# Performance work log

Hardware: AMD Instinct MI355X
Metric: run time of the kernel (lower is better)

Reference implementation:

```python
import jax, jax.numpy as jnp
import numpy as np

D_MODEL = 2048
NUM_HEADS = 16
HEAD_DIM = D_MODEL // NUM_HEADS  # 128
ROPE_BASE = 10000.0
B, L = 2, 2048


def _rope_tables(seq_len, head_dim, base):
    # inv_freq over even dims; cos/sin tables of shape (seq_len, head_dim)
    inv_freq = 1.0 / (base ** (jnp.arange(0, head_dim, 2, dtype=jnp.float32) / head_dim))
    t = jnp.arange(seq_len, dtype=jnp.float32)
    freqs = jnp.einsum('l,d->ld', t, inv_freq)          # (L, head_dim/2)
    emb = jnp.concatenate([freqs, freqs], axis=-1)       # (L, head_dim)
    return jnp.cos(emb), jnp.sin(emb)


def _apply_rope(x, cos, sin):
    # x: (B, H, L, d); rotate-half convention
    d = x.shape[-1]
    x1, x2 = x[..., : d // 2], x[..., d // 2:]
    rotated = jnp.concatenate([-x2, x1], axis=-1)
    return x * cos + rotated * sin


def setup_inputs() -> dict:
    key = jax.random.key(0)
    k0, k1, k2 = jax.random.split(key, 3)
    query = jax.random.normal(k0, (B, L, D_MODEL), dtype=jnp.float32)
    W_qkv = jax.random.normal(k1, (3 * D_MODEL, D_MODEL), dtype=jnp.float32) * 0.02
    b_qkv = jnp.zeros((3 * D_MODEL,), dtype=jnp.float32)
    W_out = jax.random.normal(k2, (D_MODEL, D_MODEL), dtype=jnp.float32) * 0.02
    b_out = jnp.zeros((D_MODEL,), dtype=jnp.float32)
    return {"query": query, "W_qkv": W_qkv, "b_qkv": b_qkv, "W_out": W_out, "b_out": b_out}


def reference(query, W_qkv, b_qkv, W_out, b_out):
    Bq, Lq, _ = query.shape
    # fused QKV projection (single matmul)
    qkv = jnp.einsum('bld,ed->ble', query, W_qkv) + b_qkv  # (B, L, 3D)
    q, k, v = jnp.split(qkv, 3, axis=-1)

    def shape_heads(x):
        return x.reshape(Bq, Lq, NUM_HEADS, HEAD_DIM).transpose(0, 2, 1, 3)  # (B,H,L,d)

    q, k, v = shape_heads(q), shape_heads(k), shape_heads(v)

    cos, sin = _rope_tables(Lq, HEAD_DIM, ROPE_BASE)
    q = _apply_rope(q, cos, sin)
    k = _apply_rope(k, cos, sin)

    scale = 1.0 / jnp.sqrt(jnp.asarray(HEAD_DIM, dtype=q.dtype))
    scores = jnp.einsum('bhqd,bhkd->bhqk', q, k) * scale  # (B,H,L,L)
    causal = jnp.tril(jnp.ones((Lq, Lq), dtype=bool))
    scores = jnp.where(causal, scores, jnp.finfo(scores.dtype).min)
    probs = jax.nn.softmax(scores, axis=-1)
    attn = jnp.einsum('bhqk,bhkd->bhqd', probs, v)        # (B,H,L,d)

    out = attn.transpose(0, 2, 1, 3).reshape(Bq, Lq, D_MODEL)
    return jnp.einsum('bld,ed->ble', out, W_out) + b_out
```

## Files before the change

### kernel.cpp

```cpp
#include <hip/hip_runtime.h>

typedef unsigned short u16;
typedef unsigned int u32;
typedef __bf16 bf16x8 __attribute__((ext_vector_type(8)));
typedef float f32x4 __attribute__((ext_vector_type(4)));

__device__ __forceinline__ u16 f2b(float f) {
  u32 u = __float_as_uint(f);
  u32 r = (u + 0x7fffu + ((u >> 16) & 1u)) >> 16;
  return (u16)r;
}
__device__ __forceinline__ float b2f(u16 v) {
  return __uint_as_float(((u32)v) << 16);
}

__global__ __launch_bounds__(256) void convert_f32_bf16(
    const float4* __restrict__ in, ushort4* __restrict__ out, int n4) {
  int i = blockIdx.x * 256 + threadIdx.x;
  if (i >= n4) return;
  float4 f = in[i];
  ushort4 o;
  o.x = f2b(f.x); o.y = f2b(f.y); o.z = f2b(f.z); o.w = f2b(f.w);
  out[i] = o;
}

template <int OUT_BF16>
__global__ __launch_bounds__(256) void gemm_bt(
    const u16* __restrict__ A, const u16* __restrict__ B,
    const float* __restrict__ bias, void* __restrict__ Cv,
    int M, int N, int K) {
  __shared__ __align__(16) u16 As[128 * 32];
  __shared__ __align__(16) u16 Bs[128 * 32];
  const int tid = threadIdx.x;
  const int lane = tid & 63;
  const int wave = tid >> 6;
  const int m0 = blockIdx.y * 128;
  const int n0 = blockIdx.x * 128;
  const int wm = (wave & 1) * 64;
  const int wn = (wave >> 1) * 64;
  f32x4 acc[4][4] = {};

  const int sr = lane >> 2, sc = lane & 3;
  const int cs = ((sc - (sr >> 1)) & 3) * 16;
  const int srow0 = wave * 32 + sr;
  const int fr = lane & 15;
  const int g = lane >> 4;
  const int fco = ((g + (fr >> 1)) & 3) * 8;

  const int kiters = K >> 5;
  for (int kt = 0; kt < kiters; ++kt) {
    const int k0 = kt << 5;
    __syncthreads();
    {
      const char* gA0 = (const char*)A + ((size_t)(m0 + srow0) * K + k0) * 2 + cs;
      const char* gA1 = gA0 + (size_t)16 * K * 2;
      const char* gB0 = (const char*)B + ((size_t)(n0 + srow0) * K + k0) * 2 + cs;
      const char* gB1 = gB0 + (size_t)16 * K * 2;
      __builtin_amdgcn_global_load_lds(
          (__attribute__((address_space(1))) void*)gA0,
          (__attribute__((address_space(3))) void*)(As + (wave * 2 + 0) * 512), 16, 0, 0);
      __builtin_amdgcn_global_load_lds(
          (__attribute__((address_space(1))) void*)gA1,
          (__attribute__((address_space(3))) void*)(As + (wave * 2 + 1) * 512), 16, 0, 0);
      __builtin_amdgcn_global_load_lds(
          (__attribute__((address_space(1))) void*)gB0,
          (__attribute__((address_space(3))) void*)(Bs + (wave * 2 + 0) * 512), 16, 0, 0);
      __builtin_amdgcn_global_load_lds(
          (__attribute__((address_space(1))) void*)gB1,
          (__attribute__((address_space(3))) void*)(Bs + (wave * 2 + 1) * 512), 16, 0, 0);
    }
    __syncthreads();
    bf16x8 aF[4], bF[4];
#pragma unroll
    for (int mi = 0; mi < 4; ++mi)
      __builtin_memcpy(&aF[mi], &As[(wm + mi * 16 + fr) * 32 + fco], 16);
#pragma unroll
    for (int ni = 0; ni < 4; ++ni)
      __builtin_memcpy(&bF[ni], &Bs[(wn + ni * 16 + fr) * 32 + fco], 16);
#pragma unroll
    for (int mi = 0; mi < 4; ++mi)
#pragma unroll
      for (int ni = 0; ni < 4; ++ni)
        acc[mi][ni] = __builtin_amdgcn_mfma_f32_16x16x32_bf16(aF[mi], bF[ni], acc[mi][ni], 0, 0, 0);
  }
  const int rq = (lane >> 4) * 4;
  const int cq = lane & 15;
#pragma unroll
  for (int mi = 0; mi < 4; ++mi) {
#pragma unroll
    for (int ni = 0; ni < 4; ++ni) {
      int col = n0 + wn + ni * 16 + cq;
      float bs = bias[col];
#pragma unroll
      for (int i = 0; i < 4; ++i) {
        int row = m0 + wm + mi * 16 + rq + i;
        float v = acc[mi][ni][i] + bs;
        if (OUT_BF16)
          ((u16*)Cv)[(size_t)row * N + col] = f2b(v);
        else
          ((float*)Cv)[(size_t)row * N + col] = v;
      }
    }
  }
}

__global__ __launch_bounds__(256) void rope_reshape(
    const u16* __restrict__ qkv, u16* __restrict__ qh, u16* __restrict__ kh) {
  int idx = blockIdx.x * 256 + threadIdx.x;
  int i = idx & 63;
  int h = (idx >> 6) & 15;
  int l = (idx >> 10) & 2047;
  int b = idx >> 21;
  const u16* row = qkv + ((size_t)(b * 2048 + l)) * 6144;
  int off = h * 128 + i;
  float q1 = b2f(row[off]), q2 = b2f(row[off + 64]);
  float k1 = b2f(row[2048 + off]), k2 = b2f(row[2048 + off + 64]);
  float inv = exp2f(-(float)i * 0.20762050593046869f);
  float ang = (float)l * inv;
  float s, c;
  sincosf(ang, &s, &c);
  size_t o = ((size_t)(b * 16 + h) * 2048 + l) * 128;
  const float qs = 0.08838834764831845f;
  qh[o + i]      = f2b((q1 * c - q2 * s) * qs);
  qh[o + 64 + i] = f2b((q2 * c + q1 * s) * qs);
  kh[o + i]      = f2b(k1 * c - k2 * s);
  kh[o + 64 + i] = f2b(k2 * c + k1 * s);
}

__global__ __launch_bounds__(256) void transpose_v(
    const u16* __restrict__ qkv, u16* __restrict__ vhT) {
  __shared__ u16 Ts[64 * 65];
  const int tid = threadIdx.x;
  const int lt = blockIdx.x;
  const int dh = blockIdx.y;
  const int bh = blockIdx.z;
  const int b = bh >> 4, h = bh & 15;
  const int l0 = lt * 64, d0 = dh * 64;
#pragma unroll
  for (int it = 0; it < 16; ++it) {
    int idx = it * 256 + tid;
    int l = idx >> 6, d = idx & 63;
    Ts[l * 65 + d] =
        qkv[((size_t)(b * 2048 + l0 + l)) * 6144 + 4096 + h * 128 + d0 + d];
  }
  __syncthreads();
#pragma unroll
  for (int it = 0; it < 16; ++it) {
    int idx = it * 256 + tid;
    int d = idx >> 6, l = idx & 63;
    vhT[((size_t)bh * 128 + d0 + d) * 2048 + l0 + l] = Ts[l * 65 + d];
  }
}

__global__ __launch_bounds__(256, 2) void attn_flash(
    const u16* __restrict__ qh, const u16* __restrict__ kh,
    const u16* __restrict__ vhT, u16* __restrict__ oh) {
  __shared__ __align__(16) u16 Ks[64 * 128];
  __shared__ __align__(16) u16 Vt[128 * 64];
  __shared__ __align__(16) u16 Ps[128 * 72];
  const int tid = threadIdx.x;
  const int lane = tid & 63;
  const int w = tid >> 6;
  const int cq = lane & 15;
  const int g = lane >> 4;
  const int p = blockIdx.x;
  const int bh = blockIdx.y;
  const int b = bh >> 4, h = bh & 15;
  const int ktiles = 32 - p;
  int q0s[2];
  q0s[0] = p * 64;
  q0s[1] = (31 - p) * 64;

  bf16x8 qf[2][4];
#pragma unroll
  for (int s = 0; s < 2; ++s) {
    const u16* qp = qh + ((size_t)bh * 2048 + q0s[s] + w * 16 + cq) * 128 + g * 8;
#pragma unroll
    for (int ks = 0; ks < 4; ++ks)
      __builtin_memcpy(&qf[s][ks], qp + ks * 32, 16);
  }

  f32x4 o[2][8] = {};
  float mrow[2] = {-1e30f, -1e30f};
  float lrow[2] = {0.0f, 0.0f};

  const int krl = lane >> 4;
  const int kcl = lane & 15;
  const int vrl = lane >> 3;
  const int vcl = lane & 7;

  for (int kt = 0; kt < ktiles; ++kt) {
    __syncthreads();
    {
      const size_t kvb = (size_t)bh * 2048 + (size_t)kt * 64;
#pragma unroll
      for (int i = 0; i < 4; ++i) {
        int row = w * 16 + i * 4 + krl;
        int cgl = kcl ^ (row & 7);
        const char* src = (const char*)(kh + (kvb + row) * 128 + cgl * 8);
        __builtin_amdgcn_global_load_lds(
            (__attribute__((address_space(1))) void*)src,
            (__attribute__((address_space(3))) void*)(Ks + (w * 16 + i * 4) * 128),
            16, 0, 0);
      }
#pragma unroll
      for (int i = 0; i < 4; ++i) {
        int row = w * 32 + i * 8 + vrl;
        int cgl = vcl ^ (row & 7);
        const char* src =
            (const char*)(vhT + ((size_t)bh * 128 + row) * 2048 + kt * 64 + cgl * 8);
        __builtin_amdgcn_global_load_lds(
            (__attribute__((address_space(1))) void*)src,
            (__attribute__((address_space(3))) void*)(Vt + (w * 32 + i * 8) * 64),
            16, 0, 0);
      }
    }
    __syncthreads();

    const bool nA = (kt <= p);
    f32x4 S[4][2] = {};
#pragma unroll
    for (int ks = 0; ks < 4; ++ks) {
#pragma unroll
      for (int mt = 0; mt < 4; ++mt) {
        bf16x8 kf;
        int slot = (ks * 4 + g) ^ (cq & 7);
        __builtin_memcpy(&kf, &Ks[(mt * 16 + cq) * 128 + slot * 8], 16);
        if (nA)
          S[mt][0] = __builtin_amdgcn_mfma_f32_16x16x32_bf16(kf, qf[0][ks], S[mt][0], 0, 0, 0);
        S[mt][1] = __builtin_amdgcn_mfma_f32_16x16x32_bf16(kf, qf[1][ks], S[mt][1], 0, 0, 0);
      }
    }

#pragma unroll
    for (int s = 0; s < 2; ++s) {
      if (s == 0 && !nA) continue;
      const int dtile = s ? (ktiles - 1) : p;
      if (kt == dtile) {
        const int qg = q0s[s] + w * 16 + cq;
#pragma unroll
        for (int mt = 0; mt < 4; ++mt)
#pragma unroll
          for (int i = 0; i < 4; ++i)
            if (kt * 64 + mt * 16 + g * 4 + i > qg) S[mt][s][i] = -1e30f;
      }
      float mx = S[0][s][0];
#pragma unroll
      for (int mt = 0; mt < 4; ++mt)
#pragma unroll
        for (int i = 0; i < 4; ++i) mx = fmaxf(mx, S[mt][s][i]);
      mx = fmaxf(mx, __shfl_xor(mx, 16));
      mx = fmaxf(mx, __shfl_xor(mx, 32));
      float mnew = fmaxf(mrow[s], mx);
      float al = __expf(mrow[s] - mnew);
      mrow[s] = mnew;
      float rs = 0.0f;
#pragma unroll
      for (int mt = 0; mt < 4; ++mt) {
        float e0 = __expf(S[mt][s][0] - mnew);
        float e1 = __expf(S[mt][s][1] - mnew);
        float e2 = __expf(S[mt][s][2] - mnew);
        float e3 = __expf(S[mt][s][3] - mnew);
        rs += (e0 + e1) + (e2 + e3);
        ushort4 pk;
        pk.x = f2b(e0); pk.y = f2b(e1); pk.z = f2b(e2); pk.w = f2b(e3);
        *(ushort4*)&Ps[(s * 64 + w * 16 + cq) * 72 + mt * 16 + g * 4] = pk;
      }
      rs += __shfl_xor(rs, 16);
      rs += __shfl_xor(rs, 32);
      lrow[s] = lrow[s] * al + rs;
#pragma unroll
      for (int dmt = 0; dmt < 8; ++dmt) {
        o[s][dmt][0] *= al; o[s][dmt][1] *= al;
        o[s][dmt][2] *= al; o[s][dmt][3] *= al;
      }
    }

#pragma unroll
    for (int ks = 0; ks < 2; ++ks) {
      bf16x8 pf0, pf1;
      if (nA) __builtin_memcpy(&pf0, &Ps[(w * 16 + cq) * 72 + ks * 32 + g * 8], 16);
      __builtin_memcpy(&pf1, &Ps[(64 + w * 16 + cq) * 72 + ks * 32 + g * 8], 16);
#pragma unroll
      for (int dmt = 0; dmt < 8; ++dmt) {
        bf16x8 vf;
        int slot = (ks * 4 + g) ^ (cq & 7);
        __builtin_memcpy(&vf, &Vt[(dmt * 16 + cq) * 64 + slot * 8], 16);
        if (nA)
          o[0][dmt] = __builtin_amdgcn_mfma_f32_16x16x32_bf16(vf, pf0, o[0][dmt], 0, 0, 0);
        o[1][dmt] = __builtin_amdgcn_mfma_f32_16x16x32_bf16(vf, pf1, o[1][dmt], 0, 0, 0);
      }
    }
  }

#pragma unroll
  for (int s = 0; s < 2; ++s) {
    float inv = 1.0f / lrow[s];
    int qg = q0s[s] + w * 16 + cq;
    size_t base = ((size_t)(b * 2048 + qg)) * 2048 + h * 128;
#pragma unroll
    for (int dmt = 0; dmt < 8; ++dmt) {
      ushort4 t;
      t.x = f2b(o[s][dmt][0] * inv);
      t.y = f2b(o[s][dmt][1] * inv);
      t.z = f2b(o[s][dmt][2] * inv);
      t.w = f2b(o[s][dmt][3] * inv);
      *(ushort4*)(oh + base + dmt * 16 + g * 4) = t;
    }
  }
}

extern "C" void kernel_launch(void* const* d_in, const int* in_sizes, int n_in,
                              void* d_out, int out_size, void* d_ws, size_t ws_size,
                              hipStream_t stream) {
  (void)in_sizes; (void)n_in; (void)out_size; (void)ws_size;
  const float* query = (const float*)d_in[0];
  const float* W_qkv = (const float*)d_in[1];
  const float* b_qkv = (const float*)d_in[2];
  const float* W_out = (const float*)d_in[3];
  const float* b_out = (const float*)d_in[4];
  float* out = (float*)d_out;
  char* ws = (char*)d_ws;

  u16* Abf  = (u16*)(ws + 0);
  u16* W1bf = (u16*)(ws + (size_t)16777216);
  u16* W2bf = (u16*)(ws + (size_t)41943040);
  u16* QKV  = (u16*)(ws + (size_t)50331648);
  u16* qhp  = (u16*)(ws + (size_t)100663296);
  u16* khp  = (u16*)(ws + (size_t)117440512);
  u16* vhT  = (u16*)(ws + (size_t)134217728);
  u16* ohp  = (u16*)(ws + (size_t)150994944);

  convert_f32_bf16<<<8192, 256, 0, stream>>>((const float4*)query, (ushort4*)Abf, 2097152);
  convert_f32_bf16<<<12288, 256, 0, stream>>>((const float4*)W_qkv, (ushort4*)W1bf, 3145728);
  convert_f32_bf16<<<4096, 256, 0, stream>>>((const float4*)W_out, (ushort4*)W2bf, 1048576);
  gemm_bt<1><<<dim3(48, 32), 256, 0, stream>>>(Abf, W1bf, b_qkv, (void*)QKV, 4096, 6144, 2048);
  rope_reshape<<<16384, 256, 0, stream>>>(QKV, qhp, khp);
  transpose_v<<<dim3(32, 2, 32), 256, 0, stream>>>(QKV, vhT);
  attn_flash<<<dim3(16, 32), 256, 0, stream>>>(qhp, khp, vhT, ohp);
  gemm_bt<0><<<dim3(16, 32), 256, 0, stream>>>(ohp, W2bf, b_out, (void*)out, 4096, 2048, 2048);
}
```

Measured before the change: 413.7 us.

## Double GEMM K-tile to 64 with XOR swizzle and merge conversion kernels

The GEMM now stages a 64-wide K slice per iteration instead of 32, so there are half as many barrier-separated load/compute rounds. LDS placement uses an XOR swizzle to avoid bank conflicts, and each staged tile feeds two MFMA sub-steps. LDS use doubles to 32 KB per block, which may lower occupancy. Separately, the three fp32-to-bf16 conversion launches are merged into one kernel that writes contiguously into the workspace, saving two launches.

```diff
diff --git a/kernel.cpp b/kernel.cpp
--- a/kernel.cpp
+++ b/kernel.cpp
@@ -14,11 +14,14 @@
   return __uint_as_float(((u32)v) << 16);
 }
 
-__global__ __launch_bounds__(256) void convert_f32_bf16(
-    const float4* __restrict__ in, ushort4* __restrict__ out, int n4) {
+__global__ __launch_bounds__(256) void convert_all(
+    const float4* __restrict__ q, const float4* __restrict__ w1,
+    const float4* __restrict__ w2, ushort4* __restrict__ out) {
   int i = blockIdx.x * 256 + threadIdx.x;
-  if (i >= n4) return;
-  float4 f = in[i];
+  float4 f;
+  if (i < 2097152) f = q[i];
+  else if (i < 5242880) f = w1[i - 2097152];
+  else f = w2[i - 5242880];
   ushort4 o;
   o.x = f2b(f.x); o.y = f2b(f.y); o.z = f2b(f.z); o.w = f2b(f.w);
   out[i] = o;
@@ -29,8 +32,8 @@
     const u16* __restrict__ A, const u16* __restrict__ B,
     const float* __restrict__ bias, void* __restrict__ Cv,
     int M, int N, int K) {
-  __shared__ __align__(16) u16 As[128 * 32];
-  __shared__ __align__(16) u16 Bs[128 * 32];
+  __shared__ __align__(16) u16 As[128 * 64];
+  __shared__ __align__(16) u16 Bs[128 * 64];
   const int tid = threadIdx.x;
   const int lane = tid & 63;
   const int wave = tid >> 6;
@@ -40,48 +43,47 @@
   const int wn = (wave >> 1) * 64;
   f32x4 acc[4][4] = {};
 
-  const int sr = lane >> 2, sc = lane & 3;
-  const int cs = ((sc - (sr >> 1)) & 3) * 16;
-  const int srow0 = wave * 32 + sr;
+  const int srow = wave * 32 + (lane >> 3);
+  const int scb = ((lane & 7) ^ (lane >> 3)) * 16;
   const int fr = lane & 15;
   const int g = lane >> 4;
-  const int fco = ((g + (fr >> 1)) & 3) * 8;
-
-  const int kiters = K >> 5;
+
+  const int kiters = K >> 6;
   for (int kt = 0; kt < kiters; ++kt) {
-    const int k0 = kt << 5;
+    const int k0 = kt << 6;
     __syncthreads();
     {
-      const char* gA0 = (const char*)A + ((size_t)(m0 + srow0) * K + k0) * 2 + cs;
-      const char* gA1 = gA0 + (size_t)16 * K * 2;
-      const char* gB0 = (const char*)B + ((size_t)(n0 + srow0) * K + k0) * 2 + cs;
-      const char* gB1 = gB0 + (size_t)16 * K * 2;
-      __builtin_amdgcn_global_load_lds(
-          (__attribute__((address_space(1))) void*)gA0,
-          (__attribute__((address_space(3))) void*)(As + (wave * 2 + 0) * 512), 16, 0, 0);
-      __builtin_amdgcn_global_load_lds(
-          (__attribute__((address_space(1))) void*)gA1,
-          (__attribute__((address_space(3))) void*)(As + (wave * 2 + 1) * 512), 16, 0, 0);
-      __builtin_amdgcn_global_load_lds(
-          (__attribute__((address_space(1))) void*)gB0,
-          (__attribute__((address_space(3))) void*)(Bs + (wave * 2 + 0) * 512), 16, 0, 0);
-      __builtin_amdgcn_global_load_lds(
-          (__attribute__((address_space(1))) void*)gB1,
-          (__attribute__((address_space(3))) void*)(Bs + (wave * 2 + 1) * 512), 16, 0, 0);
+      const char* gA = (const char*)A + ((size_t)(m0 + srow) * K + k0) * 2 + scb;
+      const char* gB = (const char*)B + ((size_t)(n0 + srow) * K + k0) * 2 + scb;
+#pragma unroll
+      for (int i = 0; i < 4; ++i) {
+        __builtin_amdgcn_global_load_lds(
+            (__attribute__((address_space(1))) void*)(gA + (size_t)i * 8 * K * 2),
+            (__attribute__((address_space(3))) void*)(As + (wave * 32 + i * 8) * 64),
+            16, 0, 0);
+        __builtin_amdgcn_global_load_lds(
+            (__attribute__((address_space(1))) void*)(gB + (size_t)i * 8 * K * 2),
+            (__attribute__((address_space(3))) void*)(Bs + (wave * 32 + i * 8) * 64),
+            16, 0, 0);
+      }
     }
     __syncthreads();
-    bf16x8 aF[4], bF[4];
-#pragma unroll
-    for (int mi = 0; mi < 4; ++mi)
-      __builtin_memcpy(&aF[mi], &As[(wm + mi * 16 + fr) * 32 + fco], 16);
-#pragma unroll
-    for (int ni = 0; ni < 4; ++ni)
-      __builtin_memcpy(&bF[ni], &Bs[(wn + ni * 16 + fr) * 32 + fco], 16);
-#pragma unroll
-    for (int mi = 0; mi < 4; ++mi)
+#pragma unroll
+    for (int ks = 0; ks < 2; ++ks) {
+      const int so = ((ks * 4 + g) ^ (fr & 7)) * 8;
+      bf16x8 aF[4], bF[4];
+#pragma unroll
+      for (int mi = 0; mi < 4; ++mi)
+        __builtin_memcpy(&aF[mi], &As[(wm + mi * 16 + fr) * 64 + so], 16);
 #pragma unroll
       for (int ni = 0; ni < 4; ++ni)
-        acc[mi][ni] = __builtin_amdgcn_mfma_f32_16x16x32_bf16(aF[mi], bF[ni], acc[mi][ni], 0, 0, 0);
+        __builtin_memcpy(&bF[ni], &Bs[(wn + ni * 16 + fr) * 64 + so], 16);
+#pragma unroll
+      for (int mi = 0; mi < 4; ++mi)
+#pragma unroll
+        for (int ni = 0; ni < 4; ++ni)
+          acc[mi][ni] = __builtin_amdgcn_mfma_f32_16x16x32_bf16(aF[mi], bF[ni], acc[mi][ni], 0, 0, 0);
+    }
   }
   const int rq = (lane >> 4) * 4;
   const int cq = lane & 15;
@@ -331,9 +333,8 @@
   u16* vhT  = (u16*)(ws + (size_t)134217728);
   u16* ohp  = (u16*)(ws + (size_t)150994944);
 
-  convert_f32_bf16<<<8192, 256, 0, stream>>>((const float4*)query, (ushort4*)Abf, 2097152);
-  convert_f32_bf16<<<12288, 256, 0, stream>>>((const float4*)W_qkv, (ushort4*)W1bf, 3145728);
-  convert_f32_bf16<<<4096, 256, 0, stream>>>((const float4*)W_out, (ushort4*)W2bf, 1048576);
+  convert_all<<<24576, 256, 0, stream>>>((const float4*)query, (const float4*)W_qkv,
+                                         (const float4*)W_out, (ushort4*)ws);
   gemm_bt<1><<<dim3(48, 32), 256, 0, stream>>>(Abf, W1bf, b_qkv, (void*)QKV, 4096, 6144, 2048);
   rope_reshape<<<16384, 256, 0, stream>>>(QKV, qhp, khp);
   transpose_v<<<dim3(32, 2, 32), 256, 0, stream>>>(QKV, vhT);
```

New measurement: 386.2 us. -6.6%, faster.
